# Optimization experiments

Hardware: AMD Instinct MI355X
Metric: run time of the kernel (lower is better)

Reference implementation:

```python
import jax, jax.numpy as jnp
import numpy as np

N = 8192
IN_F = 256
OUT_F = 256


def setup_inputs() -> dict:
    key = jax.random.key(0)
    k_v, k_adj, k1, k2, k3, kb = jax.random.split(key, 6)
    stdv = 1.0 / np.sqrt(OUT_F)
    V = jax.random.normal(k_v, (N, IN_F), dtype=jnp.float32)
    adj = jax.random.randint(k_adj, (N, N), 0, 4, dtype=jnp.int32)
    w1 = jax.random.uniform(k1, (IN_F, OUT_F), jnp.float32, -stdv, stdv)
    w2 = jax.random.uniform(k2, (IN_F, OUT_F), jnp.float32, -stdv, stdv)
    w3 = jax.random.uniform(k3, (IN_F, OUT_F), jnp.float32, -stdv, stdv)
    bias = jax.random.uniform(kb, (OUT_F,), jnp.float32, -stdv, stdv)
    return {"V": V, "adj": adj, "w1": w1, "w2": w2, "w3": w3, "bias": bias}


def reference(V, adj, w1, w2, w3, bias):
    # typed relational GCN: for each edge type k in {1,2,3},
    # aggregate (adj==k) @ (V @ wk), then sum and add bias
    o1 = jnp.matmul((adj == 1).astype(jnp.float32), jnp.matmul(V, w1))
    o2 = jnp.matmul((adj == 2).astype(jnp.float32), jnp.matmul(V, w2))
    o3 = jnp.matmul((adj == 3).astype(jnp.float32), jnp.matmul(V, w3))
    return o1 + o2 + o3 + bias
```

## Files before the change

kernel.cpp:

```cpp
#include <hip/hip_runtime.h>

typedef __attribute__((ext_vector_type(4))) float f32x4;
typedef __attribute__((ext_vector_type(16))) float f32x16;
typedef __attribute__((ext_vector_type(4))) unsigned short u16x4;
typedef __attribute__((ext_vector_type(4))) int i32x4;
typedef __attribute__((ext_vector_type(8))) __bf16 bf16x8;

union FragAB {
  u16x4 u[2];
  i32x4 v;
  bf16x8 f;
};

static __device__ __forceinline__ unsigned short f2bf(float x) {
  union { float f; unsigned u; } v;
  v.f = x;
  unsigned r = v.u + 0x7FFFu + ((v.u >> 16) & 1u);
  return (unsigned short)(r >> 16);
}

#define NN 8192

__global__ __launch_bounds__(256) void k_prep(const int* __restrict__ adj,
                                              const float* __restrict__ bias,
                                              unsigned* __restrict__ adj2,
                                              float* __restrict__ out) {
  int t = blockIdx.x * 256 + threadIdx.x;
  int nT = gridDim.x * 256;
  for (int g = t; g < 4194304; g += nT) {
    const int* p = adj + (size_t)g * 16;
    i32x4 a0 = *(const i32x4*)(p);
    i32x4 a1 = *(const i32x4*)(p + 4);
    i32x4 a2 = *(const i32x4*)(p + 8);
    i32x4 a3 = *(const i32x4*)(p + 12);
    unsigned w = (unsigned)(a0.x & 3)        | ((unsigned)(a0.y & 3) << 2)  |
                 ((unsigned)(a0.z & 3) << 4) | ((unsigned)(a0.w & 3) << 6)  |
                 ((unsigned)(a1.x & 3) << 8) | ((unsigned)(a1.y & 3) << 10) |
                 ((unsigned)(a1.z & 3) << 12)| ((unsigned)(a1.w & 3) << 14) |
                 ((unsigned)(a2.x & 3) << 16)| ((unsigned)(a2.y & 3) << 18) |
                 ((unsigned)(a2.z & 3) << 20)| ((unsigned)(a2.w & 3) << 22) |
                 ((unsigned)(a3.x & 3) << 24)| ((unsigned)(a3.y & 3) << 26) |
                 ((unsigned)(a3.z & 3) << 28)| ((unsigned)(a3.w & 3) << 30);
    adj2[g] = w;
  }
  for (int g = t; g < 524288; g += nT) {
    *(f32x4*)(out + (size_t)g * 4) = *(const f32x4*)(bias + ((g * 4) & 255));
  }
}

__global__ __launch_bounds__(256) void k_transform(
    const float* __restrict__ V, const float* __restrict__ w1,
    const float* __restrict__ w2, const float* __restrict__ w3,
    unsigned short* __restrict__ Bp) {
  int bx = blockIdx.x;
  int rb = bx & 63;
  int nb = bx >> 6;
  const float* W = (nb < 4) ? w1 : (nb < 8) ? w2 : w3;
  int nc0 = (nb & 3) * 64;
  int tid = threadIdx.x;
  int lane = tid & 63;
  int wv = tid >> 6;
  int wm = wv >> 1, wn = wv & 1;
  int q = lane >> 4, l16 = lane & 15;

  __shared__ unsigned short tA[128][36];
  __shared__ unsigned short tB[64][36];

  f32x4 acc[4][2];
#pragma unroll
  for (int i = 0; i < 4; i++)
#pragma unroll
    for (int j = 0; j < 2; j++) acc[i][j] = (f32x4)0.0f;

  for (int kk = 0; kk < 256; kk += 32) {
    {
      int r = tid >> 1, c0 = (tid & 1) * 16;
      const float* src = V + (size_t)(rb * 128 + r) * 256 + kk + c0;
      f32x4 f0 = *(const f32x4*)(src + 0);
      f32x4 f1 = *(const f32x4*)(src + 4);
      f32x4 f2 = *(const f32x4*)(src + 8);
      f32x4 f3 = *(const f32x4*)(src + 12);
      unsigned short* d = &tA[r][c0];
      d[0] = f2bf(f0.x);  d[1] = f2bf(f0.y);  d[2] = f2bf(f0.z);  d[3] = f2bf(f0.w);
      d[4] = f2bf(f1.x);  d[5] = f2bf(f1.y);  d[6] = f2bf(f1.z);  d[7] = f2bf(f1.w);
      d[8] = f2bf(f2.x);  d[9] = f2bf(f2.y);  d[10] = f2bf(f2.z); d[11] = f2bf(f2.w);
      d[12] = f2bf(f3.x); d[13] = f2bf(f3.y); d[14] = f2bf(f3.z); d[15] = f2bf(f3.w);
    }
    {
      int r = tid >> 3, c0 = (tid & 7) * 8;
      const float* src = W + (size_t)(kk + r) * 256 + nc0 + c0;
      f32x4 g0 = *(const f32x4*)(src);
      f32x4 g1 = *(const f32x4*)(src + 4);
      tB[c0 + 0][r] = f2bf(g0.x); tB[c0 + 1][r] = f2bf(g0.y);
      tB[c0 + 2][r] = f2bf(g0.z); tB[c0 + 3][r] = f2bf(g0.w);
      tB[c0 + 4][r] = f2bf(g1.x); tB[c0 + 5][r] = f2bf(g1.y);
      tB[c0 + 6][r] = f2bf(g1.z); tB[c0 + 7][r] = f2bf(g1.w);
    }
    __syncthreads();
    FragAB af[4], bf[2];
#pragma unroll
    for (int mt = 0; mt < 4; mt++) {
      const unsigned short* p = &tA[wm * 64 + mt * 16 + l16][q * 8];
      af[mt].u[0] = *(const u16x4*)p;
      af[mt].u[1] = *(const u16x4*)(p + 4);
    }
#pragma unroll
    for (int nt = 0; nt < 2; nt++) {
      const unsigned short* p = &tB[wn * 32 + nt * 16 + l16][q * 8];
      bf[nt].u[0] = *(const u16x4*)p;
      bf[nt].u[1] = *(const u16x4*)(p + 4);
    }
#pragma unroll
    for (int mt = 0; mt < 4; mt++)
#pragma unroll
      for (int nt = 0; nt < 2; nt++)
        acc[mt][nt] = __builtin_amdgcn_mfma_f32_16x16x32_bf16(
            af[mt].f, bf[nt].f, acc[mt][nt], 0, 0, 0);
    __syncthreads();
  }
  int ty = nb >> 2;
#pragma unroll
  for (int mt = 0; mt < 4; mt++)
#pragma unroll
    for (int nt = 0; nt < 2; nt++) {
      int n = (nb & 3) * 64 + wn * 32 + nt * 16 + l16;
      int j0 = rb * 128 + wm * 64 + mt * 16 + q * 4;
      u16x4 hv;
      hv.x = f2bf(acc[mt][nt].x);
      hv.y = f2bf(acc[mt][nt].y);
      hv.z = f2bf(acc[mt][nt].z);
      hv.w = f2bf(acc[mt][nt].w);
      size_t idx = (size_t)ty * 2097152 + (size_t)(j0 >> 4) * 4096 + n * 16 + (j0 & 15);
      *(u16x4*)(Bp + idx) = hv;
    }
}

__global__ __launch_bounds__(256, 4) void k_agg(const unsigned* __restrict__ adj2,
                                                const unsigned short* __restrict__ Bp,
                                                float* __restrict__ out) {
  int bx = blockIdx.x;
  int ks = bx & 7, rb = (bx >> 3) & 63, nb = bx >> 9;
  int tid = threadIdx.x, lane = tid & 63;
  int wv = tid >> 6;
  int wm = wv >> 1, wn = wv & 1;
  int q = lane >> 5, l32 = lane & 31;
  int qsh = q << 4;

  f32x16 acc[2][2];
  acc[0][0] = (f32x16)0.0f;
  acc[0][1] = (f32x16)0.0f;
  acc[1][0] = (f32x16)0.0f;
  acc[1][1] = (f32x16)0.0f;

  const unsigned* ap0 = adj2 + (size_t)(rb * 128 + wm * 64 + l32) * 512 + ks * 64;
  const unsigned* ap1 = ap0 + 32 * 512;

  int n0 = nb * 128 + wn * 64 + l32;
  const unsigned short* bp = Bp + (size_t)ks * 262144 + (size_t)n0 * 16 + q * 8;

  unsigned long long c0 = *(const unsigned long long*)ap0;
  unsigned long long c1 = *(const unsigned long long*)ap1;

  for (int step = 0; step < 32; ++step) {
    unsigned long long nx0 = 0, nx1 = 0;
    if (step < 31) {
      nx0 = *(const unsigned long long*)(ap0 + 2 * (step + 1));
      nx1 = *(const unsigned long long*)(ap1 + 2 * (step + 1));
    }
#pragma unroll
    for (int kh = 0; kh < 2; kh++) {
      FragAB bv[3][2];
#pragma unroll
      for (int ty = 0; ty < 3; ty++)
#pragma unroll
        for (int nt = 0; nt < 2; nt++)
          bv[ty][nt].v =
              *(const i32x4*)(bp + (size_t)ty * 2097152 + kh * 4096 + nt * 512);
      unsigned w0 = (unsigned)(kh ? (c0 >> 32) : c0) >> qsh;
      unsigned w1 = (unsigned)(kh ? (c1 >> 32) : c1) >> qsh;
#pragma unroll
      for (int ty = 0; ty < 3; ty++) {
        FragAB A0, A1;
#pragma unroll
        for (int d = 0; d < 4; d++) {
          unsigned p00 = (w0 >> (4 * d)) & 3u, p01 = (w0 >> (4 * d + 2)) & 3u;
          unsigned p10 = (w1 >> (4 * d)) & 3u, p11 = (w1 >> (4 * d + 2)) & 3u;
          A0.v[d] = (int)((p00 == (unsigned)(ty + 1) ? 0x3F80u : 0u) |
                          (p01 == (unsigned)(ty + 1) ? 0x3F800000u : 0u));
          A1.v[d] = (int)((p10 == (unsigned)(ty + 1) ? 0x3F80u : 0u) |
                          (p11 == (unsigned)(ty + 1) ? 0x3F800000u : 0u));
        }
        acc[0][0] = __builtin_amdgcn_mfma_f32_32x32x16_bf16(A0.f, bv[ty][0].f,
                                                            acc[0][0], 0, 0, 0);
        acc[0][1] = __builtin_amdgcn_mfma_f32_32x32x16_bf16(A0.f, bv[ty][1].f,
                                                            acc[0][1], 0, 0, 0);
        acc[1][0] = __builtin_amdgcn_mfma_f32_32x32x16_bf16(A1.f, bv[ty][0].f,
                                                            acc[1][0], 0, 0, 0);
        acc[1][1] = __builtin_amdgcn_mfma_f32_32x32x16_bf16(A1.f, bv[ty][1].f,
                                                            acc[1][1], 0, 0, 0);
      }
    }
    bp += 8192;
    c0 = nx0;
    c1 = nx1;
  }
#pragma unroll
  for (int mt = 0; mt < 2; mt++)
#pragma unroll
    for (int nt = 0; nt < 2; nt++) {
      int col = nb * 128 + wn * 64 + nt * 32 + l32;
      int rowb = rb * 128 + wm * 64 + mt * 32 + 4 * q;
#pragma unroll
      for (int r = 0; r < 16; r++) {
        int row = rowb + (r & 3) + 8 * (r >> 2);
        atomicAdd(out + (size_t)row * 256 + col, acc[mt][nt][r]);
      }
    }
}

extern "C" void kernel_launch(void* const* d_in, const int* in_sizes, int n_in,
                              void* d_out, int out_size, void* d_ws,
                              size_t ws_size, hipStream_t stream) {
  const float* V = (const float*)d_in[0];
  const int* adj = (const int*)d_in[1];
  const float* w1 = (const float*)d_in[2];
  const float* w2 = (const float*)d_in[3];
  const float* w3 = (const float*)d_in[4];
  const float* bias = (const float*)d_in[5];
  float* out = (float*)d_out;
  unsigned short* Bp = (unsigned short*)d_ws;
  unsigned* adj2 = (unsigned*)((char*)d_ws + 0xC00000);

  k_prep<<<dim3(2048), dim3(256), 0, stream>>>(adj, bias, adj2, out);
  k_transform<<<dim3(768), dim3(256), 0, stream>>>(V, w1, w2, w3, Bp);
  k_agg<<<dim3(1024), dim3(256), 0, stream>>>(adj2, Bp, out);
}
```

Before: 533.1 us.

## Widen aggregation tile to full output width with double-buffered B fragments

The aggregation kernel now has each block cover 128 rows across all 256 output columns. Each wave holds eight 32x32 accumulators and builds its adjacency fragment once per type, reusing it across eight MFMAs. B fragments are double-buffered in registers so loads overlap the MFMAs, and the grid and occupancy bound are halved. The prep kernel now also converts V to bf16 and transposes the weights, so the transform kernel loads bf16 fragments straight from global memory with no LDS or syncs. The risks are higher register pressure at 2 blocks per SM and an uncoalesced strided transpose write in prep.

```diff
diff --git a/kernel.cpp b/kernel.cpp
--- a/kernel.cpp
+++ b/kernel.cpp
@@ -21,27 +21,40 @@
 
 #define NN 8192
 
-__global__ __launch_bounds__(256) void k_prep(const int* __restrict__ adj,
-                                              const float* __restrict__ bias,
-                                              unsigned* __restrict__ adj2,
-                                              float* __restrict__ out) {
+__global__ __launch_bounds__(256) void k_prep(
+    const int* __restrict__ adj, const float* __restrict__ V,
+    const float* __restrict__ w1, const float* __restrict__ w2,
+    const float* __restrict__ w3, const float* __restrict__ bias,
+    unsigned char* __restrict__ adj2b, unsigned short* __restrict__ Vb,
+    unsigned short* __restrict__ WbT, float* __restrict__ out) {
   int t = blockIdx.x * 256 + threadIdx.x;
   int nT = gridDim.x * 256;
-  for (int g = t; g < 4194304; g += nT) {
-    const int* p = adj + (size_t)g * 16;
-    i32x4 a0 = *(const i32x4*)(p);
-    i32x4 a1 = *(const i32x4*)(p + 4);
-    i32x4 a2 = *(const i32x4*)(p + 8);
-    i32x4 a3 = *(const i32x4*)(p + 12);
-    unsigned w = (unsigned)(a0.x & 3)        | ((unsigned)(a0.y & 3) << 2)  |
-                 ((unsigned)(a0.z & 3) << 4) | ((unsigned)(a0.w & 3) << 6)  |
-                 ((unsigned)(a1.x & 3) << 8) | ((unsigned)(a1.y & 3) << 10) |
-                 ((unsigned)(a1.z & 3) << 12)| ((unsigned)(a1.w & 3) << 14) |
-                 ((unsigned)(a2.x & 3) << 16)| ((unsigned)(a2.y & 3) << 18) |
-                 ((unsigned)(a2.z & 3) << 20)| ((unsigned)(a2.w & 3) << 22) |
-                 ((unsigned)(a3.x & 3) << 24)| ((unsigned)(a3.y & 3) << 26) |
-                 ((unsigned)(a3.z & 3) << 28)| ((unsigned)(a3.w & 3) << 30);
-    adj2[g] = w;
+  for (int g = t; g < 16777216; g += nT) {
+    i32x4 a = *(const i32x4*)(adj + (size_t)g * 4);
+    adj2b[g] = (unsigned char)((a.x & 3) | ((a.y & 3) << 2) |
+                               ((a.z & 3) << 4) | ((a.w & 3) << 6));
+  }
+  for (int g = t; g < 524288; g += nT) {
+    f32x4 f = *(const f32x4*)(V + (size_t)g * 4);
+    u16x4 h;
+    h.x = f2bf(f.x); h.y = f2bf(f.y); h.z = f2bf(f.z); h.w = f2bf(f.w);
+    *(u16x4*)(Vb + (size_t)g * 4) = h;
+  }
+  {
+    const float* ws_[1];
+    for (int e = t; e < 65536; e += nT) {
+      int k = e >> 8, n = e & 255;
+      WbT[(size_t)(0 * 256 + n) * 256 + k] = f2bf(w1[e]);
+    }
+    for (int e = t; e < 65536; e += nT) {
+      int k = e >> 8, n = e & 255;
+      WbT[(size_t)(1 * 256 + n) * 256 + k] = f2bf(w2[e]);
+    }
+    for (int e = t; e < 65536; e += nT) {
+      int k = e >> 8, n = e & 255;
+      WbT[(size_t)(2 * 256 + n) * 256 + k] = f2bf(w3[e]);
+    }
+    (void)ws_;
   }
   for (int g = t; g < 524288; g += nT) {
     *(f32x4*)(out + (size_t)g * 4) = *(const f32x4*)(bias + ((g * 4) & 255));
@@ -49,173 +62,145 @@
 }
 
 __global__ __launch_bounds__(256) void k_transform(
-    const float* __restrict__ V, const float* __restrict__ w1,
-    const float* __restrict__ w2, const float* __restrict__ w3,
+    const unsigned short* __restrict__ Vb, const unsigned short* __restrict__ WbT,
     unsigned short* __restrict__ Bp) {
   int bx = blockIdx.x;
-  int rb = bx & 63;
-  int nb = bx >> 6;
-  const float* W = (nb < 4) ? w1 : (nb < 8) ? w2 : w3;
-  int nc0 = (nb & 3) * 64;
-  int tid = threadIdx.x;
-  int lane = tid & 63;
+  int rb = bx & 127, nb = bx >> 7;
+  int tid = threadIdx.x, lane = tid & 63;
   int wv = tid >> 6;
-  int wm = wv >> 1, wn = wv & 1;
+  int wr = wv >> 1, wc = wv & 1;
   int q = lane >> 4, l16 = lane & 15;
 
-  __shared__ unsigned short tA[128][36];
-  __shared__ unsigned short tB[64][36];
-
-  f32x4 acc[4][2];
-#pragma unroll
-  for (int i = 0; i < 4; i++)
-#pragma unroll
-    for (int j = 0; j < 2; j++) acc[i][j] = (f32x4)0.0f;
-
+  f32x4 acc[2][4];
+#pragma unroll
+  for (int i = 0; i < 2; i++)
+#pragma unroll
+    for (int j = 0; j < 4; j++) acc[i][j] = (f32x4)0.0f;
+
+  int r0 = rb * 64 + wr * 32 + l16;
+  int n0 = nb * 128 + wc * 64 + l16;
+  const unsigned short* av = Vb + (size_t)r0 * 256 + q * 8;
+  const unsigned short* bv = WbT + (size_t)n0 * 256 + q * 8;
+
+#pragma unroll 2
   for (int kk = 0; kk < 256; kk += 32) {
-    {
-      int r = tid >> 1, c0 = (tid & 1) * 16;
-      const float* src = V + (size_t)(rb * 128 + r) * 256 + kk + c0;
-      f32x4 f0 = *(const f32x4*)(src + 0);
-      f32x4 f1 = *(const f32x4*)(src + 4);
-      f32x4 f2 = *(const f32x4*)(src + 8);
-      f32x4 f3 = *(const f32x4*)(src + 12);
-      unsigned short* d = &tA[r][c0];
-      d[0] = f2bf(f0.x);  d[1] = f2bf(f0.y);  d[2] = f2bf(f0.z);  d[3] = f2bf(f0.w);
-      d[4] = f2bf(f1.x);  d[5] = f2bf(f1.y);  d[6] = f2bf(f1.z);  d[7] = f2bf(f1.w);
-      d[8] = f2bf(f2.x);  d[9] = f2bf(f2.y);  d[10] = f2bf(f2.z); d[11] = f2bf(f2.w);
-      d[12] = f2bf(f3.x); d[13] = f2bf(f3.y); d[14] = f2bf(f3.z); d[15] = f2bf(f3.w);
-    }
-    {
-      int r = tid >> 3, c0 = (tid & 7) * 8;
-      const float* src = W + (size_t)(kk + r) * 256 + nc0 + c0;
-      f32x4 g0 = *(const f32x4*)(src);
-      f32x4 g1 = *(const f32x4*)(src + 4);
-      tB[c0 + 0][r] = f2bf(g0.x); tB[c0 + 1][r] = f2bf(g0.y);
-      tB[c0 + 2][r] = f2bf(g0.z); tB[c0 + 3][r] = f2bf(g0.w);
-      tB[c0 + 4][r] = f2bf(g1.x); tB[c0 + 5][r] = f2bf(g1.y);
-      tB[c0 + 6][r] = f2bf(g1.z); tB[c0 + 7][r] = f2bf(g1.w);
-    }
-    __syncthreads();
-    FragAB af[4], bf[2];
-#pragma unroll
-    for (int mt = 0; mt < 4; mt++) {
-      const unsigned short* p = &tA[wm * 64 + mt * 16 + l16][q * 8];
-      af[mt].u[0] = *(const u16x4*)p;
-      af[mt].u[1] = *(const u16x4*)(p + 4);
-    }
-#pragma unroll
-    for (int nt = 0; nt < 2; nt++) {
-      const unsigned short* p = &tB[wn * 32 + nt * 16 + l16][q * 8];
-      bf[nt].u[0] = *(const u16x4*)p;
-      bf[nt].u[1] = *(const u16x4*)(p + 4);
-    }
-#pragma unroll
-    for (int mt = 0; mt < 4; mt++)
-#pragma unroll
-      for (int nt = 0; nt < 2; nt++)
+    FragAB af[2], bf[4];
+#pragma unroll
+    for (int mt = 0; mt < 2; mt++)
+      af[mt].v = *(const i32x4*)(av + (size_t)(mt * 16) * 256 + kk);
+#pragma unroll
+    for (int nt = 0; nt < 4; nt++)
+      bf[nt].v = *(const i32x4*)(bv + (size_t)(nt * 16) * 256 + kk);
+#pragma unroll
+    for (int mt = 0; mt < 2; mt++)
+#pragma unroll
+      for (int nt = 0; nt < 4; nt++)
         acc[mt][nt] = __builtin_amdgcn_mfma_f32_16x16x32_bf16(
             af[mt].f, bf[nt].f, acc[mt][nt], 0, 0, 0);
-    __syncthreads();
-  }
-  int ty = nb >> 2;
-#pragma unroll
-  for (int mt = 0; mt < 4; mt++)
-#pragma unroll
-    for (int nt = 0; nt < 2; nt++) {
-      int n = (nb & 3) * 64 + wn * 32 + nt * 16 + l16;
-      int j0 = rb * 128 + wm * 64 + mt * 16 + q * 4;
+  }
+#pragma unroll
+  for (int mt = 0; mt < 2; mt++)
+#pragma unroll
+    for (int nt = 0; nt < 4; nt++) {
+      int n = n0 + nt * 16;
+      int ty = n >> 8, nn = n & 255;
+      int j0 = rb * 64 + wr * 32 + mt * 16 + q * 4;
       u16x4 hv;
       hv.x = f2bf(acc[mt][nt].x);
       hv.y = f2bf(acc[mt][nt].y);
       hv.z = f2bf(acc[mt][nt].z);
       hv.w = f2bf(acc[mt][nt].w);
-      size_t idx = (size_t)ty * 2097152 + (size_t)(j0 >> 4) * 4096 + n * 16 + (j0 & 15);
+      size_t idx = (size_t)ty * 2097152 + (size_t)(j0 >> 4) * 4096 + nn * 16 + (j0 & 15);
       *(u16x4*)(Bp + idx) = hv;
     }
 }
 
-__global__ __launch_bounds__(256, 4) void k_agg(const unsigned* __restrict__ adj2,
+__global__ __launch_bounds__(256, 2) void k_agg(const unsigned* __restrict__ adj2,
                                                 const unsigned short* __restrict__ Bp,
                                                 float* __restrict__ out) {
   int bx = blockIdx.x;
-  int ks = bx & 7, rb = (bx >> 3) & 63, nb = bx >> 9;
+  int ks = bx & 7, rb = bx >> 3;
   int tid = threadIdx.x, lane = tid & 63;
   int wv = tid >> 6;
-  int wm = wv >> 1, wn = wv & 1;
   int q = lane >> 5, l32 = lane & 31;
   int qsh = q << 4;
 
-  f32x16 acc[2][2];
-  acc[0][0] = (f32x16)0.0f;
-  acc[0][1] = (f32x16)0.0f;
-  acc[1][0] = (f32x16)0.0f;
-  acc[1][1] = (f32x16)0.0f;
-
-  const unsigned* ap0 = adj2 + (size_t)(rb * 128 + wm * 64 + l32) * 512 + ks * 64;
-  const unsigned* ap1 = ap0 + 32 * 512;
-
-  int n0 = nb * 128 + wn * 64 + l32;
-  const unsigned short* bp = Bp + (size_t)ks * 262144 + (size_t)n0 * 16 + q * 8;
-
-  unsigned long long c0 = *(const unsigned long long*)ap0;
-  unsigned long long c1 = *(const unsigned long long*)ap1;
+  f32x16 acc[8];
+#pragma unroll
+  for (int nt = 0; nt < 8; nt++) acc[nt] = (f32x16)0.0f;
+
+  int row = rb * 128 + wv * 32 + l32;
+  const unsigned* ap = adj2 + (size_t)row * 512 + ks * 64;
+
+  const unsigned short* bp0 = Bp + (size_t)0 * 2097152 + (size_t)ks * 262144 + l32 * 16 + q * 8;
+  const unsigned short* bp1 = bp0 + 2097152;
+  const unsigned short* bp2 = bp0 + 2 * 2097152;
+
+  unsigned long long c = *(const unsigned long long*)ap;
+
+  FragAB bvA[8], bvB[8];
+#pragma unroll
+  for (int nt = 0; nt < 8; nt++)
+    bvA[nt].v = *(const i32x4*)(bp0 + nt * 512);
 
   for (int step = 0; step < 32; ++step) {
-    unsigned long long nx0 = 0, nx1 = 0;
-    if (step < 31) {
-      nx0 = *(const unsigned long long*)(ap0 + 2 * (step + 1));
-      nx1 = *(const unsigned long long*)(ap1 + 2 * (step + 1));
-    }
-#pragma unroll
-    for (int kh = 0; kh < 2; kh++) {
-      FragAB bv[3][2];
-#pragma unroll
-      for (int ty = 0; ty < 3; ty++)
-#pragma unroll
-        for (int nt = 0; nt < 2; nt++)
-          bv[ty][nt].v =
-              *(const i32x4*)(bp + (size_t)ty * 2097152 + kh * 4096 + nt * 512);
-      unsigned w0 = (unsigned)(kh ? (c0 >> 32) : c0) >> qsh;
-      unsigned w1 = (unsigned)(kh ? (c1 >> 32) : c1) >> qsh;
-#pragma unroll
-      for (int ty = 0; ty < 3; ty++) {
-        FragAB A0, A1;
-#pragma unroll
-        for (int d = 0; d < 4; d++) {
-          unsigned p00 = (w0 >> (4 * d)) & 3u, p01 = (w0 >> (4 * d + 2)) & 3u;
-          unsigned p10 = (w1 >> (4 * d)) & 3u, p11 = (w1 >> (4 * d + 2)) & 3u;
-          A0.v[d] = (int)((p00 == (unsigned)(ty + 1) ? 0x3F80u : 0u) |
-                          (p01 == (unsigned)(ty + 1) ? 0x3F800000u : 0u));
-          A1.v[d] = (int)((p10 == (unsigned)(ty + 1) ? 0x3F80u : 0u) |
-                          (p11 == (unsigned)(ty + 1) ? 0x3F800000u : 0u));
+    unsigned long long nx = 0;
+    if (step < 31) nx = *(const unsigned long long*)(ap + 2 * (step + 1));
+#pragma unroll
+    for (int s = 0; s < 6; ++s) {
+      const int kh = s / 3, ty = s % 3;
+      if (s < 5) {
+        const int nkh = (s + 1) / 3, nty = (s + 1) % 3;
+        const unsigned short* nbp = (nty == 0) ? bp0 : (nty == 1) ? bp1 : bp2;
+#pragma unroll
+        for (int nt = 0; nt < 8; nt++) {
+          if (s & 1)
+            bvA[nt].v = *(const i32x4*)(nbp + nkh * 4096 + nt * 512);
+          else
+            bvB[nt].v = *(const i32x4*)(nbp + nkh * 4096 + nt * 512);
         }
-        acc[0][0] = __builtin_amdgcn_mfma_f32_32x32x16_bf16(A0.f, bv[ty][0].f,
-                                                            acc[0][0], 0, 0, 0);
-        acc[0][1] = __builtin_amdgcn_mfma_f32_32x32x16_bf16(A0.f, bv[ty][1].f,
-                                                            acc[0][1], 0, 0, 0);
-        acc[1][0] = __builtin_amdgcn_mfma_f32_32x32x16_bf16(A1.f, bv[ty][0].f,
-                                                            acc[1][0], 0, 0, 0);
-        acc[1][1] = __builtin_amdgcn_mfma_f32_32x32x16_bf16(A1.f, bv[ty][1].f,
-                                                            acc[1][1], 0, 0, 0);
+      } else {
+#pragma unroll
+        for (int nt = 0; nt < 8; nt++) {
+          if (s & 1)
+            bvA[nt].v = *(const i32x4*)(bp0 + 8192 + nt * 512);
+          else
+            bvB[nt].v = *(const i32x4*)(bp0 + 8192 + nt * 512);
+        }
       }
-    }
-    bp += 8192;
-    c0 = nx0;
-    c1 = nx1;
-  }
-#pragma unroll
-  for (int mt = 0; mt < 2; mt++)
-#pragma unroll
-    for (int nt = 0; nt < 2; nt++) {
-      int col = nb * 128 + wn * 64 + nt * 32 + l32;
-      int rowb = rb * 128 + wm * 64 + mt * 32 + 4 * q;
-#pragma unroll
-      for (int r = 0; r < 16; r++) {
-        int row = rowb + (r & 3) + 8 * (r >> 2);
-        atomicAdd(out + (size_t)row * 256 + col, acc[mt][nt][r]);
+      unsigned w = (unsigned)(kh ? (c >> 32) : c) >> qsh;
+      FragAB A;
+#pragma unroll
+      for (int d = 0; d < 4; d++) {
+        unsigned p0 = (w >> (4 * d)) & 3u, p1 = (w >> (4 * d + 2)) & 3u;
+        A.v[d] = (int)((p0 == (unsigned)(ty + 1) ? 0x3F80u : 0u) |
+                       (p1 == (unsigned)(ty + 1) ? 0x3F800000u : 0u));
       }
-    }
+#pragma unroll
+      for (int nt = 0; nt < 8; nt++) {
+        if (s & 1)
+          acc[nt] = __builtin_amdgcn_mfma_f32_32x32x16_bf16(A.f, bvB[nt].f,
+                                                            acc[nt], 0, 0, 0);
+        else
+          acc[nt] = __builtin_amdgcn_mfma_f32_32x32x16_bf16(A.f, bvA[nt].f,
+                                                            acc[nt], 0, 0, 0);
+      }
+    }
+    bp0 += 8192;
+    bp1 += 8192;
+    bp2 += 8192;
+    c = nx;
+  }
+#pragma unroll
+  for (int nt = 0; nt < 8; nt++) {
+    int col = nt * 32 + l32;
+    int rowb = rb * 128 + wv * 32 + 4 * q;
+#pragma unroll
+    for (int r = 0; r < 16; r++) {
+      int orow = rowb + (r & 3) + 8 * (r >> 2);
+      atomicAdd(out + (size_t)orow * 256 + col, acc[nt][r]);
+    }
+  }
 }
 
 extern "C" void kernel_launch(void* const* d_in, const int* in_sizes, int n_in,
@@ -229,9 +214,12 @@
   const float* bias = (const float*)d_in[5];
   float* out = (float*)d_out;
   unsigned short* Bp = (unsigned short*)d_ws;
-  unsigned* adj2 = (unsigned*)((char*)d_ws + 0xC00000);
-
-  k_prep<<<dim3(2048), dim3(256), 0, stream>>>(adj, bias, adj2, out);
-  k_transform<<<dim3(768), dim3(256), 0, stream>>>(V, w1, w2, w3, Bp);
-  k_agg<<<dim3(1024), dim3(256), 0, stream>>>(adj2, Bp, out);
-}
+  unsigned char* adj2b = (unsigned char*)d_ws + 0xC00000;
+  unsigned short* Vb = (unsigned short*)((char*)d_ws + 0x1C00000);
+  unsigned short* WbT = (unsigned short*)((char*)d_ws + 0x2000000);
+
+  k_prep<<<dim3(2048), dim3(256), 0, stream>>>(adj, V, w1, w2, w3, bias, adj2b,
+                                               Vb, WbT, out);
+  k_transform<<<dim3(768), dim3(256), 0, stream>>>(Vb, WbT, Bp);
+  k_agg<<<dim3(512), dim3(256), 0, stream>>>((const unsigned*)adj2b, Bp, out);
+}
```

Measured after the change: 783.2 us. +46.9%, slower.

## Widen agg tile to all 256 columns and pack adjacency per 4 elements

Applied to the files above, without the earlier changes.

The aggregation kernel now covers all 256 output columns in each block, so every wave holds 2x4 accumulator tiles. Each packed adjacency word is then read and decoded once instead of twice, and the grid is halved. The prep kernel packs 4 adjacency entries per byte with one 16-byte load per thread, replacing 16 entries per word, to improve load coalescing; the byte layout matches the old word layout on little-endian. The larger accumulator state raises register use, and launch bounds drop to 2 blocks per SIMD group, which lowers occupancy.

```diff
diff --git a/kernel.cpp b/kernel.cpp
--- a/kernel.cpp
+++ b/kernel.cpp
@@ -23,25 +23,14 @@
 
 __global__ __launch_bounds__(256) void k_prep(const int* __restrict__ adj,
                                               const float* __restrict__ bias,
-                                              unsigned* __restrict__ adj2,
+                                              unsigned char* __restrict__ adj2b,
                                               float* __restrict__ out) {
   int t = blockIdx.x * 256 + threadIdx.x;
   int nT = gridDim.x * 256;
-  for (int g = t; g < 4194304; g += nT) {
-    const int* p = adj + (size_t)g * 16;
-    i32x4 a0 = *(const i32x4*)(p);
-    i32x4 a1 = *(const i32x4*)(p + 4);
-    i32x4 a2 = *(const i32x4*)(p + 8);
-    i32x4 a3 = *(const i32x4*)(p + 12);
-    unsigned w = (unsigned)(a0.x & 3)        | ((unsigned)(a0.y & 3) << 2)  |
-                 ((unsigned)(a0.z & 3) << 4) | ((unsigned)(a0.w & 3) << 6)  |
-                 ((unsigned)(a1.x & 3) << 8) | ((unsigned)(a1.y & 3) << 10) |
-                 ((unsigned)(a1.z & 3) << 12)| ((unsigned)(a1.w & 3) << 14) |
-                 ((unsigned)(a2.x & 3) << 16)| ((unsigned)(a2.y & 3) << 18) |
-                 ((unsigned)(a2.z & 3) << 20)| ((unsigned)(a2.w & 3) << 22) |
-                 ((unsigned)(a3.x & 3) << 24)| ((unsigned)(a3.y & 3) << 26) |
-                 ((unsigned)(a3.z & 3) << 28)| ((unsigned)(a3.w & 3) << 30);
-    adj2[g] = w;
+  for (int g = t; g < 16777216; g += nT) {
+    i32x4 a = *(const i32x4*)(adj + (size_t)g * 4);
+    adj2b[g] = (unsigned char)((a.x & 3) | ((a.y & 3) << 2) |
+                               ((a.z & 3) << 4) | ((a.w & 3) << 6));
   }
   for (int g = t; g < 524288; g += nT) {
     *(f32x4*)(out + (size_t)g * 4) = *(const f32x4*)(bias + ((g * 4) & 255));
@@ -135,28 +124,34 @@
     }
 }
 
-__global__ __launch_bounds__(256, 4) void k_agg(const unsigned* __restrict__ adj2,
+__global__ __launch_bounds__(256, 2) void k_agg(const unsigned* __restrict__ adj2,
                                                 const unsigned short* __restrict__ Bp,
                                                 float* __restrict__ out) {
   int bx = blockIdx.x;
-  int ks = bx & 7, rb = (bx >> 3) & 63, nb = bx >> 9;
+  int ks = bx & 7, rb = bx >> 3;
   int tid = threadIdx.x, lane = tid & 63;
   int wv = tid >> 6;
   int wm = wv >> 1, wn = wv & 1;
   int q = lane >> 5, l32 = lane & 31;
   int qsh = q << 4;
 
-  f32x16 acc[2][2];
-  acc[0][0] = (f32x16)0.0f;
-  acc[0][1] = (f32x16)0.0f;
-  acc[1][0] = (f32x16)0.0f;
-  acc[1][1] = (f32x16)0.0f;
-
-  const unsigned* ap0 = adj2 + (size_t)(rb * 128 + wm * 64 + l32) * 512 + ks * 64;
+  f32x16 acc[2][4];
+#pragma unroll
+  for (int mt = 0; mt < 2; mt++)
+#pragma unroll
+    for (int nt = 0; nt < 4; nt++) acc[mt][nt] = (f32x16)0.0f;
+
+  int r0 = rb * 128 + wm * 64 + l32;
+  const unsigned* ap0 = adj2 + (size_t)r0 * 512 + ks * 64;
   const unsigned* ap1 = ap0 + 32 * 512;
 
-  int n0 = nb * 128 + wn * 64 + l32;
-  const unsigned short* bp = Bp + (size_t)ks * 262144 + (size_t)n0 * 16 + q * 8;
+  int nbase = (wn * 128 + l32) * 16 + q * 8;
+  const unsigned short* bb[3][2];
+#pragma unroll
+  for (int ty = 0; ty < 3; ty++)
+#pragma unroll
+    for (int kh = 0; kh < 2; kh++)
+      bb[ty][kh] = Bp + (size_t)ty * 2097152 + ((size_t)ks * 64 + kh) * 4096 + nbase;
 
   unsigned long long c0 = *(const unsigned long long*)ap0;
   unsigned long long c1 = *(const unsigned long long*)ap1;
@@ -167,17 +162,15 @@
       nx0 = *(const unsigned long long*)(ap0 + 2 * (step + 1));
       nx1 = *(const unsigned long long*)(ap1 + 2 * (step + 1));
     }
-#pragma unroll
-    for (int kh = 0; kh < 2; kh++) {
-      FragAB bv[3][2];
-#pragma unroll
-      for (int ty = 0; ty < 3; ty++)
-#pragma unroll
-        for (int nt = 0; nt < 2; nt++)
-          bv[ty][nt].v =
-              *(const i32x4*)(bp + (size_t)ty * 2097152 + kh * 4096 + nt * 512);
-      unsigned w0 = (unsigned)(kh ? (c0 >> 32) : c0) >> qsh;
-      unsigned w1 = (unsigned)(kh ? (c1 >> 32) : c1) >> qsh;
+    FragAB bv0[3][4];
+#pragma unroll
+    for (int ty = 0; ty < 3; ty++)
+#pragma unroll
+      for (int nt = 0; nt < 4; nt++)
+        bv0[ty][nt].v = *(const i32x4*)(bb[ty][0] + nt * 512);
+    {
+      unsigned w0 = (unsigned)c0 >> qsh;
+      unsigned w1 = (unsigned)c1 >> qsh;
 #pragma unroll
       for (int ty = 0; ty < 3; ty++) {
         FragAB A0, A1;
@@ -190,25 +183,57 @@
           A1.v[d] = (int)((p10 == (unsigned)(ty + 1) ? 0x3F80u : 0u) |
                           (p11 == (unsigned)(ty + 1) ? 0x3F800000u : 0u));
         }
-        acc[0][0] = __builtin_amdgcn_mfma_f32_32x32x16_bf16(A0.f, bv[ty][0].f,
-                                                            acc[0][0], 0, 0, 0);
-        acc[0][1] = __builtin_amdgcn_mfma_f32_32x32x16_bf16(A0.f, bv[ty][1].f,
-                                                            acc[0][1], 0, 0, 0);
-        acc[1][0] = __builtin_amdgcn_mfma_f32_32x32x16_bf16(A1.f, bv[ty][0].f,
-                                                            acc[1][0], 0, 0, 0);
-        acc[1][1] = __builtin_amdgcn_mfma_f32_32x32x16_bf16(A1.f, bv[ty][1].f,
-                                                            acc[1][1], 0, 0, 0);
+#pragma unroll
+        for (int nt = 0; nt < 4; nt++) {
+          acc[0][nt] = __builtin_amdgcn_mfma_f32_32x32x16_bf16(
+              A0.f, bv0[ty][nt].f, acc[0][nt], 0, 0, 0);
+          acc[1][nt] = __builtin_amdgcn_mfma_f32_32x32x16_bf16(
+              A1.f, bv0[ty][nt].f, acc[1][nt], 0, 0, 0);
+        }
       }
     }
-    bp += 8192;
+    FragAB bv1[3][4];
+#pragma unroll
+    for (int ty = 0; ty < 3; ty++)
+#pragma unroll
+      for (int nt = 0; nt < 4; nt++)
+        bv1[ty][nt].v = *(const i32x4*)(bb[ty][1] + nt * 512);
+    {
+      unsigned w0 = (unsigned)(c0 >> 32) >> qsh;
+      unsigned w1 = (unsigned)(c1 >> 32) >> qsh;
+#pragma unroll
+      for (int ty = 0; ty < 3; ty++) {
+        FragAB A0, A1;
+#pragma unroll
+        for (int d = 0; d < 4; d++) {
+          unsigned p00 = (w0 >> (4 * d)) & 3u, p01 = (w0 >> (4 * d + 2)) & 3u;
+          unsigned p10 = (w1 >> (4 * d)) & 3u, p11 = (w1 >> (4 * d + 2)) & 3u;
+          A0.v[d] = (int)((p00 == (unsigned)(ty + 1) ? 0x3F80u : 0u) |
+                          (p01 == (unsigned)(ty + 1) ? 0x3F800000u : 0u));
+          A1.v[d] = (int)((p10 == (unsigned)(ty + 1) ? 0x3F80u : 0u) |
+                          (p11 == (unsigned)(ty + 1) ? 0x3F800000u : 0u));
+        }
+#pragma unroll
+        for (int nt = 0; nt < 4; nt++) {
+          acc[0][nt] = __builtin_amdgcn_mfma_f32_32x32x16_bf16(
+              A0.f, bv1[ty][nt].f, acc[0][nt], 0, 0, 0);
+          acc[1][nt] = __builtin_amdgcn_mfma_f32_32x32x16_bf16(
+              A1.f, bv1[ty][nt].f, acc[1][nt], 0, 0, 0);
+        }
+      }
+    }
+#pragma unroll
+    for (int ty = 0; ty < 3; ty++)
+#pragma unroll
+      for (int kh = 0; kh < 2; kh++) bb[ty][kh] += 8192;
     c0 = nx0;
     c1 = nx1;
   }
 #pragma unroll
   for (int mt = 0; mt < 2; mt++)
 #pragma unroll
-    for (int nt = 0; nt < 2; nt++) {
-      int col = nb * 128 + wn * 64 + nt * 32 + l32;
+    for (int nt = 0; nt < 4; nt++) {
+      int col = wn * 128 + nt * 32 + l32;
       int rowb = rb * 128 + wm * 64 + mt * 32 + 4 * q;
 #pragma unroll
       for (int r = 0; r < 16; r++) {
@@ -229,9 +254,9 @@
   const float* bias = (const float*)d_in[5];
   float* out = (float*)d_out;
   unsigned short* Bp = (unsigned short*)d_ws;
-  unsigned* adj2 = (unsigned*)((char*)d_ws + 0xC00000);
-
-  k_prep<<<dim3(2048), dim3(256), 0, stream>>>(adj, bias, adj2, out);
+  unsigned char* adj2b = (unsigned char*)d_ws + 0xC00000;
+
+  k_prep<<<dim3(2048), dim3(256), 0, stream>>>(adj, bias, adj2b, out);
   k_transform<<<dim3(768), dim3(256), 0, stream>>>(V, w1, w2, w3, Bp);
-  k_agg<<<dim3(1024), dim3(256), 0, stream>>>(adj2, Bp, out);
-}
+  k_agg<<<dim3(512), dim3(256), 0, stream>>>((const unsigned*)adj2b, Bp, out);
+}
```

New measurement: 499.8 us. 6.2% less time.
